# Kernel tuning notes

Hardware: AMD Instinct MI355X
Metric: run time of the kernel (lower is better)

Reference implementation:

```python
import jax, jax.numpy as jnp
import numpy as np

WINDOW = 128
SOFTCLAMP = 50.0


def setup_inputs() -> dict:
    key = jax.random.key(0)
    ks = jax.random.split(key, 5)
    b, h, n, d = 1, 16, 16384, 32
    nw, w = n // WINDOW, WINDOW
    q = jax.random.normal(ks[0], (b, h, n, d), dtype=jnp.float32)
    k = jax.random.normal(ks[1], (b, h, n, d), dtype=jnp.float32)
    v = jax.random.normal(ks[2], (b, h, n, d), dtype=jnp.float32)
    mask = jnp.ones((b, n), dtype=bool)
    # windowed attention bias: [b, nw, w, 2w]
    attn_bias = jax.random.normal(ks[3], (b, nw, w, 2 * w), dtype=jnp.float32)
    # memory key/value slots: [2, h, m, d]
    memory_kv = jax.random.normal(ks[4], (2, h, 4, d), dtype=jnp.float32)
    return {"q": q, "k": k, "v": v, "mask": mask,
            "attn_bias": attn_bias, "memory_kv": memory_kv}


def _local_attn(q, k, v, mask, attn_bias, memory_kv):
    b, h, n, d = q.shape
    w = WINDOW
    pad = (w - n % w) % w
    if pad > 0:
        q = jnp.pad(q, ((0, 0), (0, 0), (0, pad), (0, 0)))
        k = jnp.pad(k, ((0, 0), (0, 0), (0, pad), (0, 0)))
        v = jnp.pad(v, ((0, 0), (0, 0), (0, pad), (0, 0)))
        mask = jnp.pad(mask, ((0, 0), (0, pad)), constant_values=False)
    np_ = q.shape[-2]
    nw = np_ // w
    scale = d ** -0.5
    qw = q.reshape(b, h, nw, w, d) * scale        # (b,h,nw,w,d)
    kw = k.reshape(b, h, nw, w, d)
    vw = v.reshape(b, h, nw, w, d)
    mw = mask.reshape(b, nw, w)
    # prepend a zero window, then concat previous + current window -> 2w keys
    kp = jnp.pad(kw, ((0, 0), (0, 0), (1, 0), (0, 0), (0, 0)))
    vp = jnp.pad(vw, ((0, 0), (0, 0), (1, 0), (0, 0), (0, 0)))
    mp = jnp.pad(mw, ((0, 0), (1, 0), (0, 0)), constant_values=False)
    k2 = jnp.concatenate([kp[:, :, :-1], kp[:, :, 1:]], axis=-2)  # (b,h,nw,2w,d)
    v2 = jnp.concatenate([vp[:, :, :-1], vp[:, :, 1:]], axis=-2)
    m2 = jnp.concatenate([mp[:, :-1], mp[:, 1:]], axis=-1)        # (b,nw,2w)
    # memory key/values, broadcast over batch and windows
    mk, mv = memory_kv[0], memory_kv[1]                            # (h,m,d)
    nm = mk.shape[-2]
    mk_b = jnp.broadcast_to(mk[None, :, None], (b, h, nw, nm, d))
    mv_b = jnp.broadcast_to(mv[None, :, None], (b, h, nw, nm, d))
    k2 = jnp.concatenate([mk_b, k2], axis=-2)                      # (b,h,nw,nm+2w,d)
    v2 = jnp.concatenate([mv_b, v2], axis=-2)
    bias = jnp.pad(attn_bias, ((0, 0), (0, 0), (0, 0), (nm, 0)))   # (b,nw,w,nm+2w)
    m2 = jnp.pad(m2, ((0, 0), (0, 0), (nm, 0)), constant_values=True)
    sim = jnp.einsum('bhnid,bhnjd->bhnij', qw, k2)                 # (b,h,nw,w,nm+2w)
    sim = sim + bias[:, None]
    sim = SOFTCLAMP * jnp.tanh(sim / SOFTCLAMP)
    neg = -jnp.finfo(sim.dtype).max
    sim = jnp.where(m2[:, None, :, None, :], sim, neg)
    attn = jax.nn.softmax(sim, axis=-1)
    out = jnp.einsum('bhnij,bhnjd->bhnid', attn, v2)
    out = out.reshape(b, h, np_, d)[..., :n, :]
    return out


def reference(q, k, v, mask, attn_bias, memory_kv):
    return _local_attn(q, k, v, mask, attn_bias, memory_kv)
```

## Files before the change

kernel.cpp:

```cpp
#include <hip/hip_runtime.h>
#include <hip/hip_bf16.h>


#define H    16
#define NTOK 16384
#define D    32
#define W    128
#define NW   128
#define NM   4

#define K_OFF  0
#define VT_OFF 17408
#define P_OFF  (17408 + 18432)
#define LDS_BYTES (P_OFF + 4096)

typedef float f32x4  __attribute__((ext_vector_type(4)));
typedef short bf16x8 __attribute__((ext_vector_type(8)));

__device__ __forceinline__ unsigned cvtpk(float lo, float hi) {
    unsigned r;
    asm("v_cvt_pk_bf16_f32 %0, %1, %2" : "=v"(r) : "v"(lo), "v"(hi));
    return r;
}
__device__ __forceinline__ float exp2_fast(float x) {
#if __has_builtin(__builtin_amdgcn_exp2f)
    return __builtin_amdgcn_exp2f(x);
#else
    return __expf(x * 0.6931471805599453f);
#endif
}

__global__ __launch_bounds__(256, 4) void attn_local_mfma3(
    const float* __restrict__ q, const float* __restrict__ k,
    const float* __restrict__ v, const float* __restrict__ bias,
    const float* __restrict__ mkv, float* __restrict__ out)
{
    __shared__ __align__(16) char smem[LDS_BYTES];
    char* Kb = smem + K_OFF;
    char* Vb = smem + VT_OFF;

    const int blk  = blockIdx.x;
    const int hh   = blk & (H - 1);
    const int wi   = blk >> 4;
    const int tid  = threadIdx.x;
    const int lane = tid & 63;
    const int wid  = tid >> 6;
    const int r    = lane & 15;
    const int g    = lane >> 4;
    const int f_r  = (r >> 1) & 3;

    for (int idx = tid; idx < 288 * 8; idx += 256) {
        const int row = idx >> 3;
        const int dg  = idx & 7;
        float4 kk, vv;
        if (row < NM) {
            kk = *(const float4*)(mkv + ((size_t)hh * NM + row) * D + dg * 4);
            vv = *(const float4*)(mkv + ((size_t)(H + hh) * NM + row) * D + dg * 4);
        } else {
            const int kkI = row - 16;
            const int gr  = (wi - 1) * W + kkI;
            const bool valid = (row >= 16) && (row < 272) && (gr >= 0);
            const int grc = valid ? gr : 0;
            const float m = valid ? 1.f : 0.f;
            float4 a = *(const float4*)(k + ((size_t)hh * NTOK + grc) * D + dg * 4);
            float4 b = *(const float4*)(v + ((size_t)hh * NTOK + grc) * D + dg * 4);
            kk.x = a.x * m; kk.y = a.y * m; kk.z = a.z * m; kk.w = a.w * m;
            vv.x = b.x * m; vv.y = b.y * m; vv.z = b.z * m; vv.w = b.w * m;
        }
        if (row < 272) {
            uint2 kd; kd.x = cvtpk(kk.x, kk.y); kd.y = cvtpk(kk.z, kk.w);
            const int slot = (dg >> 1) ^ ((row >> 1) & 3);
            *(uint2*)(Kb + row * 64 + slot * 16 + (dg & 1) * 8) = kd;
        }
        float vvA[4] = {vv.x, vv.y, vv.z, vv.w};
#pragma unroll
        for (int c2 = 0; c2 < 4; ++c2) {
            const int d = dg * 4 + c2;
            const int byteoff = (d * 576 + row * 2) ^ (((d >> 1) & 3) << 4);
            *(unsigned short*)(Vb + byteoff) = (unsigned short)cvtpk(vvA[c2], vvA[c2]);
        }
    }

    const float SC = 0.17677669529663687f;
    bf16x8 qf[2];
#pragma unroll
    for (int t = 0; t < 2; ++t) {
        const float* qp = q + ((size_t)hh * NTOK + wi * W + wid * 32 + t * 16 + r) * D + g * 8;
        float4 a = *(const float4*)qp;
        float4 b = *(const float4*)(qp + 4);
        union { bf16x8 h; unsigned u[4]; } qq;
        qq.u[0] = cvtpk(a.x * SC, a.y * SC); qq.u[1] = cvtpk(a.z * SC, a.w * SC);
        qq.u[2] = cvtpk(b.x * SC, b.y * SC); qq.u[3] = cvtpk(b.z * SC, b.w * SC);
        qf[t] = qq.h;
    }

    __syncthreads();

    char* Pb = smem + P_OFF + wid * 1024;
    const f32x4 zz = {0.f, 0.f, 0.f, 0.f};
    f32x4 oacc[2][2] = {{zz, zz}, {zz, zz}};
    float lsum[2] = {0.f, 0.f};
    const bool skip8 = (wi == 0);
    const float* brow = bias + ((size_t)wi * W + wid * 32 + r) * (2 * W);

    const float L2E = 1.4426950408889634f;
    const float B50 = -72.13475204444817f;

#pragma unroll 1
    for (int c = 0; c < 9; ++c) {
        const int vb0 = (r * 576 + c * 64 + g * 16) ^ (f_r << 4);
        const bf16x8 vf0 = *(const bf16x8*)(Vb + vb0);
        const bf16x8 vf1 = *(const bf16x8*)(Vb + vb0 + 9216);

        unsigned w[2][2][2];
#pragma unroll
        for (int jj = 0; jj < 2; ++jj) {
            const int j = 2 * c + jj;
            if (j > 16) {
                w[0][jj][0] = w[0][jj][1] = w[1][jj][0] = w[1][jj][1] = 0;
                continue;
            }
            const bf16x8 kf = *(const bf16x8*)(Kb + (j * 16 + r) * 64 + ((g ^ f_r) << 4));
            f32x4 c0 = zz, c1 = zz;
            if (j > 0) {
                c0 = *(const f32x4*)(brow + (j - 1) * 16 + g * 4);
                c1 = *(const f32x4*)(brow + 16 * (2 * W) + (j - 1) * 16 + g * 4);
            }
            f32x4 s0 = __builtin_amdgcn_mfma_f32_16x16x32_bf16(kf, qf[0], c0, 0, 0, 0);
            f32x4 s1 = __builtin_amdgcn_mfma_f32_16x16x32_bf16(kf, qf[1], c1, 0, 0, 0);
            const bool masked = (j == 0 && g > 0) || (skip8 && j >= 1 && j <= 8);
            const float mres = masked ? -1e30f : B50;
            float p0[4], p1[4];
#pragma unroll
            for (int i = 0; i < 4; ++i) {
                float s  = s0[i];
                float ss = s * 0.02f, u = ss * ss;
                float wv = __builtin_fmaf(u, 0.13333333333f, -0.33333333333f);
                float w2 = __builtin_fmaf(u, wv, 1.0f);
                p0[i] = exp2_fast(__builtin_fmaf(s * w2, L2E, mres));
                lsum[0] += p0[i];
                s  = s1[i];
                ss = s * 0.02f; u = ss * ss;
                wv = __builtin_fmaf(u, 0.13333333333f, -0.33333333333f);
                w2 = __builtin_fmaf(u, wv, 1.0f);
                p1[i] = exp2_fast(__builtin_fmaf(s * w2, L2E, mres));
                lsum[1] += p1[i];
            }
            w[0][jj][0] = cvtpk(p0[0], p0[1]); w[0][jj][1] = cvtpk(p0[2], p0[3]);
            w[1][jj][0] = cvtpk(p1[0], p1[1]); w[1][jj][1] = cvtpk(p1[2], p1[3]);
        }

#pragma unroll
        for (int t = 0; t < 2; ++t) {
            uint2 w0; w0.x = w[t][0][0]; w0.y = w[t][0][1];
            uint2 w1; w1.x = w[t][1][0]; w1.y = w[t][1][1];
            *(uint2*)(Pb + r * 64 + (((g >> 1) ^ f_r) << 4) + (g & 1) * 8) = w0;
            *(uint2*)(Pb + r * 64 + (((2 + (g >> 1)) ^ f_r) << 4) + (g & 1) * 8) = w1;
            const bf16x8 pa = *(const bf16x8*)(Pb + r * 64 + ((g ^ f_r) << 4));
            oacc[t][0] = __builtin_amdgcn_mfma_f32_16x16x32_bf16(pa, vf0, oacc[t][0], 0, 0, 0);
            oacc[t][1] = __builtin_amdgcn_mfma_f32_16x16x32_bf16(pa, vf1, oacc[t][1], 0, 0, 0);
        }
    }

#pragma unroll
    for (int t = 0; t < 2; ++t) {
        lsum[t] += __shfl_xor(lsum[t], 16, 64);
        lsum[t] += __shfl_xor(lsum[t], 32, 64);
    }
#pragma unroll
    for (int t = 0; t < 2; ++t) {
#pragma unroll
        for (int i = 0; i < 4; ++i) {
            const int qi = g * 4 + i;
            const float dn  = __shfl(lsum[t], qi, 64);
            const float rdn = __builtin_amdgcn_rcpf(dn);
            const size_t orow = ((size_t)hh * NTOK + wi * W + wid * 32 + t * 16 + qi) * D;
            out[orow + r]      = oacc[t][0][i] * rdn;
            out[orow + 16 + r] = oacc[t][1][i] * rdn;
        }
    }
}

extern "C" void kernel_launch(void* const* d_in, const int* in_sizes, int n_in,
                              void* d_out, int out_size, void* d_ws, size_t ws_size,
                              hipStream_t stream)
{
    const float* q    = (const float*)d_in[0];
    const float* k    = (const float*)d_in[1];
    const float* v    = (const float*)d_in[2];
    const float* bias = (const float*)d_in[4];
    const float* mkv  = (const float*)d_in[5];
    float* out = (float*)d_out;

    hipLaunchKernelGGL(attn_local_mfma3, dim3(NW * H), dim3(256), 0, stream,
                       q, k, v, bias, mkv, out);
}
```

Measured before the change: 57.98 us.

## Software-pipeline K/V/bias loads and batch staging loads in local attention

```diff
diff --git a/kernel.cpp b/kernel.cpp
--- a/kernel.cpp
+++ b/kernel.cpp
@@ -10,8 +10,8 @@
 #define NM   4
 
 #define K_OFF  0
-#define VT_OFF 17408
-#define P_OFF  (17408 + 18432)
+#define VT_OFF 18432
+#define P_OFF  (18432 + 18432)
 #define LDS_BYTES (P_OFF + 4096)
 
 typedef float f32x4  __attribute__((ext_vector_type(4)));
@@ -30,7 +30,7 @@
 #endif
 }
 
-__global__ __launch_bounds__(256, 4) void attn_local_mfma3(
+__global__ __launch_bounds__(256, 4) void attn_local_mfma5(
     const float* __restrict__ q, const float* __restrict__ k,
     const float* __restrict__ v, const float* __restrict__ bias,
     const float* __restrict__ mkv, float* __restrict__ out)
@@ -49,35 +49,43 @@
     const int g    = lane >> 4;
     const int f_r  = (r >> 1) & 3;
 
-    for (int idx = tid; idx < 288 * 8; idx += 256) {
-        const int row = idx >> 3;
-        const int dg  = idx & 7;
-        float4 kk, vv;
-        if (row < NM) {
-            kk = *(const float4*)(mkv + ((size_t)hh * NM + row) * D + dg * 4);
-            vv = *(const float4*)(mkv + ((size_t)(H + hh) * NM + row) * D + dg * 4);
-        } else {
-            const int kkI = row - 16;
-            const int gr  = (wi - 1) * W + kkI;
-            const bool valid = (row >= 16) && (row < 272) && (gr >= 0);
-            const int grc = valid ? gr : 0;
-            const float m = valid ? 1.f : 0.f;
-            float4 a = *(const float4*)(k + ((size_t)hh * NTOK + grc) * D + dg * 4);
-            float4 b = *(const float4*)(v + ((size_t)hh * NTOK + grc) * D + dg * 4);
-            kk.x = a.x * m; kk.y = a.y * m; kk.z = a.z * m; kk.w = a.w * m;
-            vv.x = b.x * m; vv.y = b.y * m; vv.z = b.z * m; vv.w = b.w * m;
-        }
-        if (row < 272) {
-            uint2 kd; kd.x = cvtpk(kk.x, kk.y); kd.y = cvtpk(kk.z, kk.w);
+#pragma unroll
+    for (int it = 0; it < 3; ++it) {
+        float4 ka[3], va[3];
+        int rows[3], dgs[3];
+#pragma unroll
+        for (int u = 0; u < 3; ++u) {
+            const int idx = tid + (it * 3 + u) * 256;
+            const int row = idx >> 3;
+            const int dg  = idx & 7;
+            rows[u] = row; dgs[u] = dg;
+            if (row < NM) {
+                ka[u] = *(const float4*)(mkv + ((size_t)hh * NM + row) * D + dg * 4);
+                va[u] = *(const float4*)(mkv + ((size_t)(H + hh) * NM + row) * D + dg * 4);
+            } else {
+                const int gr = (wi - 1) * W + (row - 16);
+                const bool valid = (row >= 16) && (row < 272) && (gr >= 0);
+                const int grc = valid ? gr : 0;
+                float4 a = *(const float4*)(k + ((size_t)hh * NTOK + grc) * D + dg * 4);
+                float4 b = *(const float4*)(v + ((size_t)hh * NTOK + grc) * D + dg * 4);
+                const float m = valid ? 1.f : 0.f;
+                ka[u].x = a.x * m; ka[u].y = a.y * m; ka[u].z = a.z * m; ka[u].w = a.w * m;
+                va[u].x = b.x * m; va[u].y = b.y * m; va[u].z = b.z * m; va[u].w = b.w * m;
+            }
+        }
+#pragma unroll
+        for (int u = 0; u < 3; ++u) {
+            const int row = rows[u], dg = dgs[u];
+            uint2 kd; kd.x = cvtpk(ka[u].x, ka[u].y); kd.y = cvtpk(ka[u].z, ka[u].w);
             const int slot = (dg >> 1) ^ ((row >> 1) & 3);
             *(uint2*)(Kb + row * 64 + slot * 16 + (dg & 1) * 8) = kd;
-        }
-        float vvA[4] = {vv.x, vv.y, vv.z, vv.w};
-#pragma unroll
-        for (int c2 = 0; c2 < 4; ++c2) {
-            const int d = dg * 4 + c2;
-            const int byteoff = (d * 576 + row * 2) ^ (((d >> 1) & 3) << 4);
-            *(unsigned short*)(Vb + byteoff) = (unsigned short)cvtpk(vvA[c2], vvA[c2]);
+            float vvA[4] = {va[u].x, va[u].y, va[u].z, va[u].w};
+#pragma unroll
+            for (int c2 = 0; c2 < 4; ++c2) {
+                const int d = dg * 4 + c2;
+                const int byteoff = (d * 576 + row * 2) ^ (((d >> 1) & 3) << 4);
+                *(unsigned short*)(Vb + byteoff) = (unsigned short)cvtpk(vvA[c2], vvA[c2]);
+            }
         }
     }
 
@@ -99,55 +107,78 @@
     char* Pb = smem + P_OFF + wid * 1024;
     const f32x4 zz = {0.f, 0.f, 0.f, 0.f};
     f32x4 oacc[2][2] = {{zz, zz}, {zz, zz}};
-    float lsum[2] = {0.f, 0.f};
+    f32x4 lsum4[2] = {zz, zz};
     const bool skip8 = (wi == 0);
     const float* brow = bias + ((size_t)wi * W + wid * 32 + r) * (2 * W);
 
     const float L2E = 1.4426950408889634f;
     const float B50 = -72.13475204444817f;
 
+    #define LDK(j)  (*(const bf16x8*)(Kb + ((j) * 16 + r) * 64 + ((g ^ f_r) << 4)))
+    #define LDV0(c) (*(const bf16x8*)(Vb + ((r * 576 + (c) * 64 + g * 16) ^ (f_r << 4))))
+    #define LDV1(c) (*(const bf16x8*)(Vb + 9216 + ((r * 576 + (c) * 64 + g * 16) ^ (f_r << 4))))
+
+    bf16x8 kfA = LDK(0), kfB = LDK(1);
+    bf16x8 vf0 = LDV0(0), vf1 = LDV1(0);
+    f32x4 bA0 = zz, bA1 = zz;
+    f32x4 bB0 = *(const f32x4*)(brow + g * 4);
+    f32x4 bB1 = *(const f32x4*)(brow + 4096 + g * 4);
+
 #pragma unroll 1
     for (int c = 0; c < 9; ++c) {
-        const int vb0 = (r * 576 + c * 64 + g * 16) ^ (f_r << 4);
-        const bf16x8 vf0 = *(const bf16x8*)(Vb + vb0);
-        const bf16x8 vf1 = *(const bf16x8*)(Vb + vb0 + 9216);
+        const int jA = 2 * c + 2, jB = 2 * c + 3;
+        bf16x8 n_kfA = LDK(jA > 17 ? 17 : jA), n_kfB = LDK(jB > 17 ? 17 : jB);
+        bf16x8 n_vf0 = LDV0(c < 8 ? c + 1 : 8), n_vf1 = LDV1(c < 8 ? c + 1 : 8);
+        const int offA = (jA <= 16) ? (jA - 1) * 16 : 0;
+        const int offB = (jB <= 16) ? (jB - 1) * 16 : 0;
+        f32x4 nA0 = *(const f32x4*)(brow + offA + g * 4);
+        f32x4 nA1 = *(const f32x4*)(brow + 4096 + offA + g * 4);
+        f32x4 nB0 = *(const f32x4*)(brow + offB + g * 4);
+        f32x4 nB1 = *(const f32x4*)(brow + 4096 + offB + g * 4);
+
+        f32x4 sA0 = __builtin_amdgcn_mfma_f32_16x16x32_bf16(kfA, qf[0], bA0, 0, 0, 0);
+        f32x4 sA1 = __builtin_amdgcn_mfma_f32_16x16x32_bf16(kfA, qf[1], bA1, 0, 0, 0);
+        f32x4 sB0 = __builtin_amdgcn_mfma_f32_16x16x32_bf16(kfB, qf[0], bB0, 0, 0, 0);
+        f32x4 sB1 = __builtin_amdgcn_mfma_f32_16x16x32_bf16(kfB, qf[1], bB1, 0, 0, 0);
+
+        const bool mA = (c == 0 && g > 0) || (skip8 && c >= 1 && c <= 4);
+        const bool mB = (skip8 && c <= 3) || (c == 8);
+        const float mresA = mA ? -1e30f : B50;
+        const float mresB = mB ? -1e30f : B50;
 
         unsigned w[2][2][2];
-#pragma unroll
-        for (int jj = 0; jj < 2; ++jj) {
-            const int j = 2 * c + jj;
-            if (j > 16) {
-                w[0][jj][0] = w[0][jj][1] = w[1][jj][0] = w[1][jj][1] = 0;
-                continue;
+        {
+            float pA0[4], pA1[4], pB0[4], pB1[4];
+#pragma unroll
+            for (int i = 0; i < 4; ++i) {
+                float s, ss, u, wv, w2;
+                s = sA0[i]; ss = s * 0.02f; u = ss * ss;
+                wv = __builtin_fmaf(u, 0.13333333333f, -0.33333333333f);
+                w2 = __builtin_fmaf(u, wv, 1.0f);
+                pA0[i] = exp2_fast(__builtin_fmaf(s * w2, L2E, mresA));
+                s = sA1[i]; ss = s * 0.02f; u = ss * ss;
+                wv = __builtin_fmaf(u, 0.13333333333f, -0.33333333333f);
+                w2 = __builtin_fmaf(u, wv, 1.0f);
+                pA1[i] = exp2_fast(__builtin_fmaf(s * w2, L2E, mresA));
+                s = sB0[i]; ss = s * 0.02f; u = ss * ss;
+                wv = __builtin_fmaf(u, 0.13333333333f, -0.33333333333f);
+                w2 = __builtin_fmaf(u, wv, 1.0f);
+                pB0[i] = exp2_fast(__builtin_fmaf(s * w2, L2E, mresB));
+                s = sB1[i]; ss = s * 0.02f; u = ss * ss;
+                wv = __builtin_fmaf(u, 0.13333333333f, -0.33333333333f);
+                w2 = __builtin_fmaf(u, wv, 1.0f);
+                pB1[i] = exp2_fast(__builtin_fmaf(s * w2, L2E, mresB));
             }
-            const bf16x8 kf = *(const bf16x8*)(Kb + (j * 16 + r) * 64 + ((g ^ f_r) << 4));
-            f32x4 c0 = zz, c1 = zz;
-            if (j > 0) {
-                c0 = *(const f32x4*)(brow + (j - 1) * 16 + g * 4);
-                c1 = *(const f32x4*)(brow + 16 * (2 * W) + (j - 1) * 16 + g * 4);
-            }
-            f32x4 s0 = __builtin_amdgcn_mfma_f32_16x16x32_bf16(kf, qf[0], c0, 0, 0, 0);
-            f32x4 s1 = __builtin_amdgcn_mfma_f32_16x16x32_bf16(kf, qf[1], c1, 0, 0, 0);
-            const bool masked = (j == 0 && g > 0) || (skip8 && j >= 1 && j <= 8);
-            const float mres = masked ? -1e30f : B50;
-            float p0[4], p1[4];
-#pragma unroll
-            for (int i = 0; i < 4; ++i) {
-                float s  = s0[i];
-                float ss = s * 0.02f, u = ss * ss;
-                float wv = __builtin_fmaf(u, 0.13333333333f, -0.33333333333f);
-                float w2 = __builtin_fmaf(u, wv, 1.0f);
-                p0[i] = exp2_fast(__builtin_fmaf(s * w2, L2E, mres));
-                lsum[0] += p0[i];
-                s  = s1[i];
-                ss = s * 0.02f; u = ss * ss;
-                wv = __builtin_fmaf(u, 0.13333333333f, -0.33333333333f);
-                w2 = __builtin_fmaf(u, wv, 1.0f);
-                p1[i] = exp2_fast(__builtin_fmaf(s * w2, L2E, mres));
-                lsum[1] += p1[i];
-            }
-            w[0][jj][0] = cvtpk(p0[0], p0[1]); w[0][jj][1] = cvtpk(p0[2], p0[3]);
-            w[1][jj][0] = cvtpk(p1[0], p1[1]); w[1][jj][1] = cvtpk(p1[2], p1[3]);
+            f32x4 a0 = {pA0[0], pA0[1], pA0[2], pA0[3]};
+            f32x4 a1 = {pA1[0], pA1[1], pA1[2], pA1[3]};
+            f32x4 b0 = {pB0[0], pB0[1], pB0[2], pB0[3]};
+            f32x4 b1 = {pB1[0], pB1[1], pB1[2], pB1[3]};
+            lsum4[0] += a0 + b0;
+            lsum4[1] += a1 + b1;
+            w[0][0][0] = cvtpk(pA0[0], pA0[1]); w[0][0][1] = cvtpk(pA0[2], pA0[3]);
+            w[1][0][0] = cvtpk(pA1[0], pA1[1]); w[1][0][1] = cvtpk(pA1[2], pA1[3]);
+            w[0][1][0] = cvtpk(pB0[0], pB0[1]); w[0][1][1] = cvtpk(pB0[2], pB0[3]);
+            w[1][1][0] = cvtpk(pB1[0], pB1[1]); w[1][1][1] = cvtpk(pB1[2], pB1[3]);
         }
 
 #pragma unroll
@@ -160,10 +191,15 @@
             oacc[t][0] = __builtin_amdgcn_mfma_f32_16x16x32_bf16(pa, vf0, oacc[t][0], 0, 0, 0);
             oacc[t][1] = __builtin_amdgcn_mfma_f32_16x16x32_bf16(pa, vf1, oacc[t][1], 0, 0, 0);
         }
-    }
-
+
+        kfA = n_kfA; kfB = n_kfB; vf0 = n_vf0; vf1 = n_vf1;
+        bA0 = nA0; bA1 = nA1; bB0 = nB0; bB1 = nB1;
+    }
+
+    float lsum[2];
 #pragma unroll
     for (int t = 0; t < 2; ++t) {
+        lsum[t] = (lsum4[t][0] + lsum4[t][1]) + (lsum4[t][2] + lsum4[t][3]);
         lsum[t] += __shfl_xor(lsum[t], 16, 64);
         lsum[t] += __shfl_xor(lsum[t], 32, 64);
     }
@@ -192,6 +228,6 @@
     const float* mkv  = (const float*)d_in[5];
     float* out = (float*)d_out;
 
-    hipLaunchKernelGGL(attn_local_mfma3, dim3(NW * H), dim3(256), 0, stream,
+    hipLaunchKernelGGL(attn_local_mfma5, dim3(NW * H), dim3(256), 0, stream,
                        q, k, v, bias, mkv, out);
 }
```

New measurement: 57.62 us. About the same (-0.6%).

## Use 8 waves per window, one 16-row tile each, shuffle P instead of LDS

Applied to the files above, without the earlier changes.

```diff
diff --git a/kernel.cpp b/kernel.cpp
--- a/kernel.cpp
+++ b/kernel.cpp
@@ -9,10 +9,8 @@
 #define NW   128
 #define NM   4
 
-#define K_OFF  0
 #define VT_OFF 17408
-#define P_OFF  (17408 + 18432)
-#define LDS_BYTES (P_OFF + 4096)
+#define LDS_BYTES (17408 + 18432)
 
 typedef float f32x4  __attribute__((ext_vector_type(4)));
 typedef short bf16x8 __attribute__((ext_vector_type(8)));
@@ -30,13 +28,13 @@
 #endif
 }
 
-__global__ __launch_bounds__(256, 4) void attn_local_mfma3(
+__global__ __launch_bounds__(512, 6) void attn_local_mfma6(
     const float* __restrict__ q, const float* __restrict__ k,
     const float* __restrict__ v, const float* __restrict__ bias,
     const float* __restrict__ mkv, float* __restrict__ out)
 {
     __shared__ __align__(16) char smem[LDS_BYTES];
-    char* Kb = smem + K_OFF;
+    char* Kb = smem;
     char* Vb = smem + VT_OFF;
 
     const int blk  = blockIdx.x;
@@ -49,30 +47,29 @@
     const int g    = lane >> 4;
     const int f_r  = (r >> 1) & 3;
 
-    for (int idx = tid; idx < 288 * 8; idx += 256) {
+    for (int idx = tid; idx < 288 * 8; idx += 512) {
         const int row = idx >> 3;
         const int dg  = idx & 7;
-        float4 kk, vv;
+        float4 ka, va;
         if (row < NM) {
-            kk = *(const float4*)(mkv + ((size_t)hh * NM + row) * D + dg * 4);
-            vv = *(const float4*)(mkv + ((size_t)(H + hh) * NM + row) * D + dg * 4);
+            ka = *(const float4*)(mkv + ((size_t)hh * NM + row) * D + dg * 4);
+            va = *(const float4*)(mkv + ((size_t)(H + hh) * NM + row) * D + dg * 4);
         } else {
-            const int kkI = row - 16;
-            const int gr  = (wi - 1) * W + kkI;
+            const int gr = (wi - 1) * W + (row - 16);
             const bool valid = (row >= 16) && (row < 272) && (gr >= 0);
             const int grc = valid ? gr : 0;
-            const float m = valid ? 1.f : 0.f;
             float4 a = *(const float4*)(k + ((size_t)hh * NTOK + grc) * D + dg * 4);
             float4 b = *(const float4*)(v + ((size_t)hh * NTOK + grc) * D + dg * 4);
-            kk.x = a.x * m; kk.y = a.y * m; kk.z = a.z * m; kk.w = a.w * m;
-            vv.x = b.x * m; vv.y = b.y * m; vv.z = b.z * m; vv.w = b.w * m;
+            const float m = valid ? 1.f : 0.f;
+            ka.x = a.x * m; ka.y = a.y * m; ka.z = a.z * m; ka.w = a.w * m;
+            va.x = b.x * m; va.y = b.y * m; va.z = b.z * m; va.w = b.w * m;
         }
         if (row < 272) {
-            uint2 kd; kd.x = cvtpk(kk.x, kk.y); kd.y = cvtpk(kk.z, kk.w);
+            uint2 kd; kd.x = cvtpk(ka.x, ka.y); kd.y = cvtpk(ka.z, ka.w);
             const int slot = (dg >> 1) ^ ((row >> 1) & 3);
             *(uint2*)(Kb + row * 64 + slot * 16 + (dg & 1) * 8) = kd;
         }
-        float vvA[4] = {vv.x, vv.y, vv.z, vv.w};
+        float vvA[4] = {va.x, va.y, va.z, va.w};
 #pragma unroll
         for (int c2 = 0; c2 < 4; ++c2) {
             const int d = dg * 4 + c2;
@@ -82,102 +79,107 @@
     }
 
     const float SC = 0.17677669529663687f;
-    bf16x8 qf[2];
-#pragma unroll
-    for (int t = 0; t < 2; ++t) {
-        const float* qp = q + ((size_t)hh * NTOK + wi * W + wid * 32 + t * 16 + r) * D + g * 8;
+    bf16x8 qf;
+    {
+        const float* qp = q + ((size_t)hh * NTOK + wi * W + wid * 16 + r) * D + g * 8;
         float4 a = *(const float4*)qp;
         float4 b = *(const float4*)(qp + 4);
         union { bf16x8 h; unsigned u[4]; } qq;
         qq.u[0] = cvtpk(a.x * SC, a.y * SC); qq.u[1] = cvtpk(a.z * SC, a.w * SC);
         qq.u[2] = cvtpk(b.x * SC, b.y * SC); qq.u[3] = cvtpk(b.z * SC, b.w * SC);
-        qf[t] = qq.h;
+        qf = qq.h;
     }
 
     __syncthreads();
 
-    char* Pb = smem + P_OFF + wid * 1024;
     const f32x4 zz = {0.f, 0.f, 0.f, 0.f};
-    f32x4 oacc[2][2] = {{zz, zz}, {zz, zz}};
-    float lsum[2] = {0.f, 0.f};
+    f32x4 oacc[2] = {zz, zz};
+    f32x4 lsum4 = zz;
     const bool skip8 = (wi == 0);
-    const float* brow = bias + ((size_t)wi * W + wid * 32 + r) * (2 * W);
+    const float* brow = bias + ((size_t)wi * W + wid * 16 + r) * (2 * W);
 
     const float L2E = 1.4426950408889634f;
     const float B50 = -72.13475204444817f;
 
+    #define LDK(j)  (*(const bf16x8*)(Kb + ((j) * 16 + r) * 64 + ((g ^ f_r) << 4)))
+    #define LDV0(c) (*(const bf16x8*)(Vb + ((r * 576 + (c) * 64 + g * 16) ^ (f_r << 4))))
+    #define LDV1(c) (*(const bf16x8*)(Vb + 9216 + ((r * 576 + (c) * 64 + g * 16) ^ (f_r << 4))))
+
+    const int idxLo = r + ((g & 1) << 5);
+    const bool hi   = (lane >= 32);
+
 #pragma unroll 1
     for (int c = 0; c < 9; ++c) {
-        const int vb0 = (r * 576 + c * 64 + g * 16) ^ (f_r << 4);
-        const bf16x8 vf0 = *(const bf16x8*)(Vb + vb0);
-        const bf16x8 vf1 = *(const bf16x8*)(Vb + vb0 + 9216);
+        const int jB = (c < 8) ? (2 * c + 1) : 16;
+        const bf16x8 kfA = LDK(2 * c);
+        const bf16x8 kfB = LDK(jB);
+        const bf16x8 vf0 = LDV0(c);
+        const bf16x8 vf1 = LDV1(c);
 
-        unsigned w[2][2][2];
+        f32x4 cA = zz;
+        if (c > 0) cA = *(const f32x4*)(brow + (2 * c - 1) * 16 + g * 4);
+        const int offB = (c < 8) ? 2 * c * 16 : 0;
+        const f32x4 cB = *(const f32x4*)(brow + offB + g * 4);
+
+        f32x4 sA = __builtin_amdgcn_mfma_f32_16x16x32_bf16(kfA, qf, cA, 0, 0, 0);
+        f32x4 sB = __builtin_amdgcn_mfma_f32_16x16x32_bf16(kfB, qf, cB, 0, 0, 0);
+
+        const bool mA = (c == 0 && g > 0) || (skip8 && c >= 1 && c <= 4);
+        const bool mB = (skip8 && c <= 3) || (c == 8);
+        const float mresA = mA ? -1e30f : B50;
+        const float mresB = mB ? -1e30f : B50;
+
+        float pA[4], pB[4];
 #pragma unroll
-        for (int jj = 0; jj < 2; ++jj) {
-            const int j = 2 * c + jj;
-            if (j > 16) {
-                w[0][jj][0] = w[0][jj][1] = w[1][jj][0] = w[1][jj][1] = 0;
-                continue;
-            }
-            const bf16x8 kf = *(const bf16x8*)(Kb + (j * 16 + r) * 64 + ((g ^ f_r) << 4));
-            f32x4 c0 = zz, c1 = zz;
-            if (j > 0) {
-                c0 = *(const f32x4*)(brow + (j - 1) * 16 + g * 4);
-                c1 = *(const f32x4*)(brow + 16 * (2 * W) + (j - 1) * 16 + g * 4);
-            }
-            f32x4 s0 = __builtin_amdgcn_mfma_f32_16x16x32_bf16(kf, qf[0], c0, 0, 0, 0);
-            f32x4 s1 = __builtin_amdgcn_mfma_f32_16x16x32_bf16(kf, qf[1], c1, 0, 0, 0);
-            const bool masked = (j == 0 && g > 0) || (skip8 && j >= 1 && j <= 8);
-            const float mres = masked ? -1e30f : B50;
-            float p0[4], p1[4];
-#pragma unroll
-            for (int i = 0; i < 4; ++i) {
-                float s  = s0[i];
-                float ss = s * 0.02f, u = ss * ss;
-                float wv = __builtin_fmaf(u, 0.13333333333f, -0.33333333333f);
-                float w2 = __builtin_fmaf(u, wv, 1.0f);
-                p0[i] = exp2_fast(__builtin_fmaf(s * w2, L2E, mres));
-                lsum[0] += p0[i];
-                s  = s1[i];
-                ss = s * 0.02f; u = ss * ss;
-                wv = __builtin_fmaf(u, 0.13333333333f, -0.33333333333f);
-                w2 = __builtin_fmaf(u, wv, 1.0f);
-                p1[i] = exp2_fast(__builtin_fmaf(s * w2, L2E, mres));
-                lsum[1] += p1[i];
-            }
-            w[0][jj][0] = cvtpk(p0[0], p0[1]); w[0][jj][1] = cvtpk(p0[2], p0[3]);
-            w[1][jj][0] = cvtpk(p1[0], p1[1]); w[1][jj][1] = cvtpk(p1[2], p1[3]);
+        for (int i = 0; i < 4; ++i) {
+            float s, ss, u, wv, w2;
+            s = sA[i]; ss = s * 0.02f; u = ss * ss;
+            wv = __builtin_fmaf(u, 0.13333333333f, -0.33333333333f);
+            w2 = __builtin_fmaf(u, wv, 1.0f);
+            pA[i] = exp2_fast(__builtin_fmaf(s * w2, L2E, mresA));
+            s = sB[i]; ss = s * 0.02f; u = ss * ss;
+            wv = __builtin_fmaf(u, 0.13333333333f, -0.33333333333f);
+            w2 = __builtin_fmaf(u, wv, 1.0f);
+            pB[i] = exp2_fast(__builtin_fmaf(s * w2, L2E, mresB));
         }
+        f32x4 a4 = {pA[0], pA[1], pA[2], pA[3]};
+        f32x4 b4 = {pB[0], pB[1], pB[2], pB[3]};
+        lsum4 += a4 + b4;
+
+        const unsigned d0 = cvtpk(pA[0], pA[1]);
+        const unsigned d1 = cvtpk(pA[2], pA[3]);
+        const unsigned d2 = cvtpk(pB[0], pB[1]);
+        const unsigned d3 = cvtpk(pB[2], pB[3]);
+        const unsigned a0 = __shfl(d0, idxLo, 64);
+        const unsigned a1 = __shfl(d1, idxLo, 64);
+        const unsigned a2 = __shfl(d2, idxLo, 64);
+        const unsigned a3 = __shfl(d3, idxLo, 64);
+        const unsigned b0 = __shfl(d0, idxLo + 16, 64);
+        const unsigned b1 = __shfl(d1, idxLo + 16, 64);
+        const unsigned b2 = __shfl(d2, idxLo + 16, 64);
+        const unsigned b3 = __shfl(d3, idxLo + 16, 64);
+        union { bf16x8 h; unsigned u[4]; } pa;
+        pa.u[0] = hi ? a2 : a0;
+        pa.u[1] = hi ? a3 : a1;
+        pa.u[2] = hi ? b2 : b0;
+        pa.u[3] = hi ? b3 : b1;
+
+        oacc[0] = __builtin_amdgcn_mfma_f32_16x16x32_bf16(pa.h, vf0, oacc[0], 0, 0, 0);
+        oacc[1] = __builtin_amdgcn_mfma_f32_16x16x32_bf16(pa.h, vf1, oacc[1], 0, 0, 0);
+    }
+
+    float lsum = (lsum4[0] + lsum4[1]) + (lsum4[2] + lsum4[3]);
+    lsum += __shfl_xor(lsum, 16, 64);
+    lsum += __shfl_xor(lsum, 32, 64);
 
 #pragma unroll
-        for (int t = 0; t < 2; ++t) {
-            uint2 w0; w0.x = w[t][0][0]; w0.y = w[t][0][1];
-            uint2 w1; w1.x = w[t][1][0]; w1.y = w[t][1][1];
-            *(uint2*)(Pb + r * 64 + (((g >> 1) ^ f_r) << 4) + (g & 1) * 8) = w0;
-            *(uint2*)(Pb + r * 64 + (((2 + (g >> 1)) ^ f_r) << 4) + (g & 1) * 8) = w1;
-            const bf16x8 pa = *(const bf16x8*)(Pb + r * 64 + ((g ^ f_r) << 4));
-            oacc[t][0] = __builtin_amdgcn_mfma_f32_16x16x32_bf16(pa, vf0, oacc[t][0], 0, 0, 0);
-            oacc[t][1] = __builtin_amdgcn_mfma_f32_16x16x32_bf16(pa, vf1, oacc[t][1], 0, 0, 0);
-        }
-    }
-
-#pragma unroll
-    for (int t = 0; t < 2; ++t) {
-        lsum[t] += __shfl_xor(lsum[t], 16, 64);
-        lsum[t] += __shfl_xor(lsum[t], 32, 64);
-    }
-#pragma unroll
-    for (int t = 0; t < 2; ++t) {
-#pragma unroll
-        for (int i = 0; i < 4; ++i) {
-            const int qi = g * 4 + i;
-            const float dn  = __shfl(lsum[t], qi, 64);
-            const float rdn = __builtin_amdgcn_rcpf(dn);
-            const size_t orow = ((size_t)hh * NTOK + wi * W + wid * 32 + t * 16 + qi) * D;
-            out[orow + r]      = oacc[t][0][i] * rdn;
-            out[orow + 16 + r] = oacc[t][1][i] * rdn;
-        }
+    for (int i = 0; i < 4; ++i) {
+        const int qi = g * 4 + i;
+        const float dn  = __shfl(lsum, qi, 64);
+        const float rdn = __builtin_amdgcn_rcpf(dn);
+        const size_t orow = ((size_t)hh * NTOK + wi * W + wid * 16 + qi) * D;
+        out[orow + r]      = oacc[0][i] * rdn;
+        out[orow + 16 + r] = oacc[1][i] * rdn;
     }
 }
 
@@ -192,6 +194,6 @@
     const float* mkv  = (const float*)d_in[5];
     float* out = (float*)d_out;
 
-    hipLaunchKernelGGL(attn_local_mfma3, dim3(NW * H), dim3(256), 0, stream,
+    hipLaunchKernelGGL(attn_local_mfma6, dim3(NW * H), dim3(512), 0, stream,
                        q, k, v, bias, mkv, out);
 }
```

Result: slower. 59.87 us (+3.3%).
